# Optimization experiments

Measured on AMD Instinct MI355X. Metric: run time of the kernel, lower is better.

## Reference

```python
import jax, jax.numpy as jnp
import numpy as np

B, S, D, H = 4, 1024, 1024, 16
DK = D // H  # 64


def setup_inputs() -> dict:
    key = jax.random.key(0)
    kx, kq, kk, kv, ko = jax.random.split(key, 5)
    scale = 1.0 / np.sqrt(D)
    x = jax.random.normal(kx, (B, S, D), dtype=jnp.float32)
    # per-head torch nn.Linear weights stacked: [H, d_k, d_model]
    Wq = jax.random.uniform(kq, (H, DK, D), jnp.float32, -scale, scale)
    Wk = jax.random.uniform(kk, (H, DK, D), jnp.float32, -scale, scale)
    Wv = jax.random.uniform(kv, (H, DK, D), jnp.float32, -scale, scale)
    Wo = jax.random.uniform(ko, (D, D), jnp.float32, -scale, scale)  # torch layout [out, in]
    # causal mask, broadcastable to (B, H, S, S); True = keep
    mask = jnp.tril(jnp.ones((S, S), dtype=bool))[None, None]
    return {"x": x, "Wq": Wq, "Wk": Wk, "Wv": Wv, "Wo": Wo, "mask": mask}


def reference(x, Wq, Wk, Wv, Wo, mask):
    # self-attention: context = x. Batched equivalent of the per-head loop.
    Q = jnp.einsum('bsd,hkd->bhsk', x, Wq)  # (B,H,S,DK)
    K = jnp.einsum('bsd,hkd->bhsk', x, Wk)
    V = jnp.einsum('bsd,hkd->bhsk', x, Wv)
    scores = jnp.einsum('bhqd,bhkd->bhqk', Q, K) / jnp.sqrt(jnp.float32(DK))
    scores = jnp.where(mask, scores, jnp.float32(-jnp.inf))
    weights = jax.nn.softmax(scores, axis=-1)  # (B,H,S,S)
    out = jnp.einsum('bhqk,bhkd->bhqd', weights, V)  # (B,H,S,DK)
    # concat heads along feature dim (head order preserved), then W_o
    concat = jnp.swapaxes(out, 1, 2).reshape(B, S, D)
    output = jnp.einsum('bqd,od->bqo', concat, Wo)
    return output, weights
```

## Files before the change

### kernel.cpp

```cpp
#include <hip/hip_runtime.h>
#include <hip/hip_bf16.h>

#define BB 4
#define SS 1024
#define DD 1024
#define HH 16
#define DKK 64

typedef __bf16 bf16;
typedef __bf16 bf16x8 __attribute__((ext_vector_type(8)));
typedef __bf16 bf16x4 __attribute__((ext_vector_type(4)));
typedef float f32x4 __attribute__((ext_vector_type(4)));

#define MFMA(a, b, c) __builtin_amdgcn_mfma_f32_16x16x32_bf16((a), (b), (c), 0, 0, 0)

__device__ __forceinline__ bf16x8 load8(const bf16* p) {
    return *reinterpret_cast<const bf16x8*>(p);
}

__device__ __forceinline__ void gload16(const bf16* g, bf16* l) {
    __builtin_amdgcn_global_load_lds(
        (const __attribute__((address_space(1))) void*)g,
        (__attribute__((address_space(3))) void*)l, 16, 0, 0);
}

__global__ __launch_bounds__(256) void cvt_bf16(const float* __restrict__ x,
                                                const float* __restrict__ Wq,
                                                const float* __restrict__ Wk,
                                                const float* __restrict__ Wv,
                                                const float* __restrict__ Wo,
                                                bf16* __restrict__ dst) {
    const size_t MEG = 1024 * 1024;
    size_t e = ((size_t)blockIdx.x * 256 + threadIdx.x) * 4;
    const float* src;
    size_t off;
    if (e < 4 * MEG)      { src = x;  off = e; }
    else if (e < 5 * MEG) { src = Wq; off = e - 4 * MEG; }
    else if (e < 6 * MEG) { src = Wk; off = e - 5 * MEG; }
    else if (e < 7 * MEG) { src = Wv; off = e - 6 * MEG; }
    else                  { src = Wo; off = e - 7 * MEG; }
    f32x4 v = *reinterpret_cast<const f32x4*>(src + off);
    bf16x4 o;
    o[0] = (bf16)v[0]; o[1] = (bf16)v[1]; o[2] = (bf16)v[2]; o[3] = (bf16)v[3];
    *reinterpret_cast<bf16x4*>(dst + e) = o;
}

template <int MODE>
__global__ __launch_bounds__(256) void gemm128(const bf16* __restrict__ A,
                                               const bf16* __restrict__ Bm,
                                               void* __restrict__ o0,
                                               void* __restrict__ o1,
                                               void* __restrict__ o2) {
    const int lane = threadIdx.x & 63;
    const int wave = threadIdx.x >> 6;
    const int wr = wave >> 1, wc = wave & 1;
    const int m0 = blockIdx.x * 128;
    const int n0 = blockIdx.y * 128;
    const int K = DD;

    __shared__ __align__(16) bf16 As[128][32];
    __shared__ __align__(16) bf16 Bs[128][32];

    const int r0 = wave * 32 + (lane >> 2);
    const int r1 = r0 + 16;
    const int csw = ((lane & 3) ^ (r0 & 3)) * 8;

    const bf16* Ag0 = A + (size_t)(m0 + r0) * K + csw;
    const bf16* Ag1 = A + (size_t)(m0 + r1) * K + csw;
    const bf16* Bg0 = Bm + (size_t)(n0 + r0) * K + csw;
    const bf16* Bg1 = Bm + (size_t)(n0 + r1) * K + csw;
    bf16* Aw0 = &As[wave * 32][0];
    bf16* Aw1 = &As[wave * 32 + 16][0];
    bf16* Bw0 = &Bs[wave * 32][0];
    bf16* Bw1 = &Bs[wave * 32 + 16][0];

    const int rsw = ((lane >> 4) ^ (lane & 3)) * 8;
    const int rrow = lane & 15;

    f32x4 acc[4][4] = {};

    for (int k0 = 0; k0 < K; k0 += 32) {
        __syncthreads();
        gload16(Ag0 + k0, Aw0);
        gload16(Ag1 + k0, Aw1);
        gload16(Bg0 + k0, Bw0);
        gload16(Bg1 + k0, Bw1);
        __syncthreads();
        bf16x8 af[4], bfr[4];
#pragma unroll
        for (int i = 0; i < 4; i++)
            af[i] = *reinterpret_cast<const bf16x8*>(&As[wr * 64 + i * 16 + rrow][rsw]);
#pragma unroll
        for (int j = 0; j < 4; j++)
            bfr[j] = *reinterpret_cast<const bf16x8*>(&Bs[wc * 64 + j * 16 + rrow][rsw]);
#pragma unroll
        for (int i = 0; i < 4; i++)
#pragma unroll
            for (int j = 0; j < 4; j++)
                acc[i][j] = MFMA(af[i], bfr[j], acc[i][j]);
    }

    if constexpr (MODE == 0) {
        bf16* Qo = (bf16*)o0;
        bf16* Ko = (bf16*)o1;
        bf16* Vto = (bf16*)o2;
        const int z = n0 >> 10;
#pragma unroll
        for (int i = 0; i < 4; i++)
#pragma unroll
            for (int j = 0; j < 4; j++)
#pragma unroll
                for (int r = 0; r < 4; r++) {
                    int m = m0 + wr * 64 + i * 16 + (lane >> 4) * 4 + r;
                    int n = n0 + wc * 64 + j * 16 + (lane & 15);
                    int b = m >> 10, s = m & 1023;
                    int nn = n & 1023, h = nn >> 6, dk = nn & 63;
                    bf16 v = (bf16)acc[i][j][r];
                    if (z == 0)
                        Qo[(((size_t)(b * HH + h)) * SS + s) * DKK + dk] = v;
                    else if (z == 1)
                        Ko[(((size_t)(b * HH + h)) * SS + s) * DKK + dk] = v;
                    else
                        Vto[(((size_t)(b * HH + h)) * DKK + dk) * SS + s] = v;
                }
    } else {
        float* Out = (float*)o0;
#pragma unroll
        for (int i = 0; i < 4; i++)
#pragma unroll
            for (int j = 0; j < 4; j++)
#pragma unroll
                for (int r = 0; r < 4; r++) {
                    int m = m0 + wr * 64 + i * 16 + (lane >> 4) * 4 + r;
                    int n = n0 + wc * 64 + j * 16 + (lane & 15);
                    Out[(size_t)m * DD + n] = acc[i][j][r];
                }
    }
}

__global__ __launch_bounds__(256, 4) void attn(const bf16* __restrict__ Q,
                                               const bf16* __restrict__ K,
                                               const bf16* __restrict__ Vt,
                                               float* __restrict__ Wgt,
                                               bf16* __restrict__ Ctx) {
    const int tid = threadIdx.x;
    const int lane = tid & 63;
    const int wave = tid >> 6;
    const int bh = blockIdx.x;
    const int qb = (blockIdx.y + (blockIdx.x & 3)) & 15;
    const int q0 = qb * 64 + wave * 16;
    const int lr = lane & 15;
    const int g = lane >> 4;
    const int lk8 = g * 8;
    const int rbase = g * 4;
    const int own_diag = q0 >> 4;
    const int nch = qb + 1;

    const bf16* Qb = Q + (size_t)bh * SS * DKK;
    const bf16* Kb = K + (size_t)bh * SS * DKK;
    const bf16* Vb = Vt + (size_t)bh * DKK * SS;
    float* Wrow = Wgt + ((size_t)bh * SS + q0) * SS;

    __shared__ __align__(16) bf16 Ks[2][64][64];
    __shared__ __align__(16) bf16 Vs[2][64][64];
    __shared__ __align__(16) bf16 Ps[4][16][40];

    const int skr = tid >> 2;
    const int sc0 = tid & 3;
    const int sw0 = (sc0 ^ (skr & 7)) * 8;
    const int sw1 = ((sc0 + 4) ^ (skr & 7)) * 8;

    bf16x8 qa0 = load8(Qb + (size_t)(q0 + lr) * DKK + lk8);
    bf16x8 qa1 = load8(Qb + (size_t)(q0 + lr) * DKK + 32 + lk8);
#pragma unroll
    for (int i = 0; i < 8; i++) {
        qa0[i] = (bf16)((float)qa0[i] * 0.125f);
        qa1[i] = (bf16)((float)qa1[i] * 0.125f);
    }

    const int rsw0 = (g ^ (lr & 7)) * 8;
    const int rsw1 = ((4 + g) ^ (lr & 7)) * 8;

    float sl[4] = {0.f, 0.f, 0.f, 0.f};

    {
        bf16x8 ka = load8(Kb + (size_t)skr * DKK + sc0 * 8);
        bf16x8 kb_ = load8(Kb + (size_t)skr * DKK + (sc0 + 4) * 8);
        *reinterpret_cast<bf16x8*>(&Ks[0][skr][sw0]) = ka;
        *reinterpret_cast<bf16x8*>(&Ks[0][skr][sw1]) = kb_;
        __syncthreads();
        for (int ch = 0; ch < nch; ch++) {
            const int cur = ch & 1;
            if (ch + 1 < nch) {
                ka = load8(Kb + (size_t)((ch + 1) * 64 + skr) * DKK + sc0 * 8);
                kb_ = load8(Kb + (size_t)((ch + 1) * 64 + skr) * DKK + (sc0 + 4) * 8);
            }
#pragma unroll
            for (int t = 0; t < 4; t++) {
                const int kt = ch * 4 + t;
                if (kt <= own_diag) {
                    bf16x8 kb0 = *reinterpret_cast<const bf16x8*>(&Ks[cur][t * 16 + lr][rsw0]);
                    bf16x8 kb1 = *reinterpret_cast<const bf16x8*>(&Ks[cur][t * 16 + lr][rsw1]);
                    f32x4 sc = {};
                    sc = MFMA(qa0, kb0, sc);
                    sc = MFMA(qa1, kb1, sc);
                    const int kcol = kt * 16 + lr;
#pragma unroll
                    for (int r = 0; r < 4; r++)
                        sl[r] += (kcol <= q0 + rbase + r) ? __expf(sc[r]) : 0.f;
                }
            }
            if (ch + 1 < nch) {
                *reinterpret_cast<bf16x8*>(&Ks[cur ^ 1][skr][sw0]) = ka;
                *reinterpret_cast<bf16x8*>(&Ks[cur ^ 1][skr][sw1]) = kb_;
            }
            __syncthreads();
        }
    }
    float inv[4];
#pragma unroll
    for (int r = 0; r < 4; r++) {
        float t = sl[r];
        t += __shfl_xor(t, 1);
        t += __shfl_xor(t, 2);
        t += __shfl_xor(t, 4);
        t += __shfl_xor(t, 8);
        inv[r] = 1.f / t;
    }

    f32x4 oacc[4] = {};
    {
        bf16x8 ka = load8(Kb + (size_t)skr * DKK + sc0 * 8);
        bf16x8 kb_ = load8(Kb + (size_t)skr * DKK + (sc0 + 4) * 8);
        bf16x8 va = load8(Vb + (size_t)skr * SS + sc0 * 8);
        bf16x8 vb_ = load8(Vb + (size_t)skr * SS + (sc0 + 4) * 8);
        *reinterpret_cast<bf16x8*>(&Ks[0][skr][sw0]) = ka;
        *reinterpret_cast<bf16x8*>(&Ks[0][skr][sw1]) = kb_;
        *reinterpret_cast<bf16x8*>(&Vs[0][skr][sw0]) = va;
        *reinterpret_cast<bf16x8*>(&Vs[0][skr][sw1]) = vb_;
        __syncthreads();
        for (int ch = 0; ch < nch; ch++) {
            const int cur = ch & 1;
            if (ch + 1 < nch) {
                ka = load8(Kb + (size_t)((ch + 1) * 64 + skr) * DKK + sc0 * 8);
                kb_ = load8(Kb + (size_t)((ch + 1) * 64 + skr) * DKK + (sc0 + 4) * 8);
                va = load8(Vb + (size_t)skr * SS + (ch + 1) * 64 + sc0 * 8);
                vb_ = load8(Vb + (size_t)skr * SS + (ch + 1) * 64 + (sc0 + 4) * 8);
            }
#pragma unroll
            for (int t = 0; t < 4; t++) {
                const int kt = ch * 4 + t;
                if (kt <= own_diag) {
                    bf16x8 kb0 = *reinterpret_cast<const bf16x8*>(&Ks[cur][t * 16 + lr][rsw0]);
                    bf16x8 kb1 = *reinterpret_cast<const bf16x8*>(&Ks[cur][t * 16 + lr][rsw1]);
                    f32x4 sc = {};
                    sc = MFMA(qa0, kb0, sc);
                    sc = MFMA(qa1, kb1, sc);
                    const int kcol = kt * 16 + lr;
#pragma unroll
                    for (int r = 0; r < 4; r++) {
                        float p = (kcol <= q0 + rbase + r) ? __expf(sc[r]) * inv[r] : 0.f;
                        Ps[wave][rbase + r][(t & 1) * 16 + lr] = (bf16)p;
                    }
                } else {
#pragma unroll
                    for (int r = 0; r < 4; r++)
                        Ps[wave][rbase + r][(t & 1) * 16 + lr] = (bf16)0.f;
                }
                if (t & 1) {
                    const int colbase = ch * 64 + (t >> 1) * 32;
                    const int prow = lane >> 2;
                    const int pcol = (lane & 3) * 8;
                    bf16x8 pv8 = *reinterpret_cast<const bf16x8*>(&Ps[wave][prow][pcol]);
                    f32x4 w0, w1;
#pragma unroll
                    for (int i = 0; i < 4; i++) {
                        w0[i] = (float)pv8[i];
                        w1[i] = (float)pv8[4 + i];
                    }
                    float* dst = Wrow + (size_t)prow * SS + colbase + pcol;
                    *reinterpret_cast<f32x4*>(dst) = w0;
                    *reinterpret_cast<f32x4*>(dst + 4) = w1;
                    if (kt - 1 <= own_diag) {
                        const int p2 = t >> 1;
                        bf16x8 pf = *reinterpret_cast<const bf16x8*>(&Ps[wave][lr][lk8]);
#pragma unroll
                        for (int j = 0; j < 4; j++) {
                            bf16x8 vb = *reinterpret_cast<const bf16x8*>(
                                &Vs[cur][j * 16 + lr][((4 * p2 + g) ^ (lr & 7)) * 8]);
                            oacc[j] = MFMA(pf, vb, oacc[j]);
                        }
                    }
                }
            }
            if (ch + 1 < nch) {
                *reinterpret_cast<bf16x8*>(&Ks[cur ^ 1][skr][sw0]) = ka;
                *reinterpret_cast<bf16x8*>(&Ks[cur ^ 1][skr][sw1]) = kb_;
                *reinterpret_cast<bf16x8*>(&Vs[cur ^ 1][skr][sw0]) = va;
                *reinterpret_cast<bf16x8*>(&Vs[cur ^ 1][skr][sw1]) = vb_;
            }
            __syncthreads();
        }
    }

    const int b = bh >> 4, h = bh & 15;
#pragma unroll
    for (int j = 0; j < 4; j++)
#pragma unroll
        for (int r = 0; r < 4; r++) {
            int qrow = q0 + rbase + r;
            int col = h * 64 + j * 16 + lr;
            Ctx[((size_t)b * SS + qrow) * DD + col] = (bf16)oacc[j][r];
        }

    const int zc0 = nch * 64;
    if (zc0 < SS) {
        const int nc4 = (SS - zc0) >> 2;
        float* zbase = Wgt + ((size_t)bh * SS + qb * 64) * SS + zc0;
        const f32x4 z = {0.f, 0.f, 0.f, 0.f};
        for (int r = 0; r < 64; r++)
            for (int c = tid; c < nc4; c += 256)
                reinterpret_cast<f32x4*>(zbase + (size_t)r * SS)[c] = z;
    }
}

extern "C" void kernel_launch(void* const* d_in, const int* in_sizes, int n_in,
                              void* d_out, int out_size, void* d_ws, size_t ws_size,
                              hipStream_t stream) {
    const float* x  = (const float*)d_in[0];
    const float* Wq = (const float*)d_in[1];
    const float* Wk = (const float*)d_in[2];
    const float* Wv = (const float*)d_in[3];
    const float* Wo = (const float*)d_in[4];

    float* out = (float*)d_out;
    float* wgt = out + (size_t)BB * SS * DD;

    const size_t MEG = 1024 * 1024;
    bf16* xb   = (bf16*)d_ws;
    bf16* wcat = xb + 4 * MEG;
    bf16* wob  = xb + 7 * MEG;
    bf16* qws  = xb + 8 * MEG;
    bf16* kws  = xb + 12 * MEG;
    bf16* vws  = xb + 16 * MEG;
    bf16* cws  = xb + 20 * MEG;

    cvt_bf16<<<dim3(8192), 256, 0, stream>>>(x, Wq, Wk, Wv, Wo, xb);
    gemm128<0><<<dim3(32, 24), 256, 0, stream>>>(xb, wcat, qws, kws, vws);
    attn<<<dim3(64, 16), 256, 0, stream>>>(qws, kws, vws, wgt, cws);
    gemm128<1><<<dim3(32, 8), 256, 0, stream>>>(cws, wob, out, nullptr, nullptr);
}
```

Before: 146.3 us.

## Double GEMM K-tile to 64 and interleave causal zero-fill with first attention pass

```diff
diff --git a/kernel.cpp b/kernel.cpp
--- a/kernel.cpp
+++ b/kernel.cpp
@@ -58,46 +58,53 @@
     const int n0 = blockIdx.y * 128;
     const int K = DD;
 
-    __shared__ __align__(16) bf16 As[128][32];
-    __shared__ __align__(16) bf16 Bs[128][32];
-
-    const int r0 = wave * 32 + (lane >> 2);
-    const int r1 = r0 + 16;
-    const int csw = ((lane & 3) ^ (r0 & 3)) * 8;
-
-    const bf16* Ag0 = A + (size_t)(m0 + r0) * K + csw;
-    const bf16* Ag1 = A + (size_t)(m0 + r1) * K + csw;
-    const bf16* Bg0 = Bm + (size_t)(n0 + r0) * K + csw;
-    const bf16* Bg1 = Bm + (size_t)(n0 + r1) * K + csw;
-    bf16* Aw0 = &As[wave * 32][0];
-    bf16* Aw1 = &As[wave * 32 + 16][0];
-    bf16* Bw0 = &Bs[wave * 32][0];
-    bf16* Bw1 = &Bs[wave * 32 + 16][0];
-
-    const int rsw = ((lane >> 4) ^ (lane & 3)) * 8;
+    __shared__ __align__(16) bf16 As[128][64];
+    __shared__ __align__(16) bf16 Bs[128][64];
+
+    const int srow = lane >> 3;
+    const int csw = ((lane & 7) ^ srow) * 8;
+
+    const bf16 *Ag[4], *Bg[4];
+    bf16 *Aw[4], *Bw[4];
+#pragma unroll
+    for (int q = 0; q < 4; q++) {
+        const int rr = wave * 32 + q * 8;
+        Ag[q] = A + (size_t)(m0 + rr + srow) * K + csw;
+        Bg[q] = Bm + (size_t)(n0 + rr + srow) * K + csw;
+        Aw[q] = &As[rr][0];
+        Bw[q] = &Bs[rr][0];
+    }
+
     const int rrow = lane & 15;
+    const int g = lane >> 4;
+    const int rs0 = (g ^ (rrow & 7)) * 8;
+    const int rs1 = ((4 + g) ^ (rrow & 7)) * 8;
 
     f32x4 acc[4][4] = {};
 
-    for (int k0 = 0; k0 < K; k0 += 32) {
+    for (int k0 = 0; k0 < K; k0 += 64) {
         __syncthreads();
-        gload16(Ag0 + k0, Aw0);
-        gload16(Ag1 + k0, Aw1);
-        gload16(Bg0 + k0, Bw0);
-        gload16(Bg1 + k0, Bw1);
+#pragma unroll
+        for (int q = 0; q < 4; q++) gload16(Ag[q] + k0, Aw[q]);
+#pragma unroll
+        for (int q = 0; q < 4; q++) gload16(Bg[q] + k0, Bw[q]);
         __syncthreads();
-        bf16x8 af[4], bfr[4];
-#pragma unroll
-        for (int i = 0; i < 4; i++)
-            af[i] = *reinterpret_cast<const bf16x8*>(&As[wr * 64 + i * 16 + rrow][rsw]);
-#pragma unroll
-        for (int j = 0; j < 4; j++)
-            bfr[j] = *reinterpret_cast<const bf16x8*>(&Bs[wc * 64 + j * 16 + rrow][rsw]);
-#pragma unroll
-        for (int i = 0; i < 4; i++)
+#pragma unroll
+        for (int half = 0; half < 2; half++) {
+            const int rs = half ? rs1 : rs0;
+            bf16x8 af[4], bfr[4];
+#pragma unroll
+            for (int i = 0; i < 4; i++)
+                af[i] = *reinterpret_cast<const bf16x8*>(&As[wr * 64 + i * 16 + rrow][rs]);
 #pragma unroll
             for (int j = 0; j < 4; j++)
-                acc[i][j] = MFMA(af[i], bfr[j], acc[i][j]);
+                bfr[j] = *reinterpret_cast<const bf16x8*>(&Bs[wc * 64 + j * 16 + rrow][rs]);
+#pragma unroll
+            for (int i = 0; i < 4; i++)
+#pragma unroll
+                for (int j = 0; j < 4; j++)
+                    acc[i][j] = MFMA(af[i], bfr[j], acc[i][j]);
+        }
     }
 
     if constexpr (MODE == 0) {
@@ -181,6 +188,14 @@
     const int rsw0 = (g ^ (lr & 7)) * 8;
     const int rsw1 = ((4 + g) ^ (lr & 7)) * 8;
 
+    const int nz4 = 256 - nch * 16;
+    const int npt = nz4 >> 2;
+    const int npc = (npt + nch - 1) / nch;
+    float* zptr = Wgt + ((size_t)bh * SS + qb * 64 + (tid >> 2)) * SS
+                + nch * 64 + (tid & 3) * 4;
+    const f32x4 z4 = {0.f, 0.f, 0.f, 0.f};
+    int zj = 0;
+
     float sl[4] = {0.f, 0.f, 0.f, 0.f};
 
     {
@@ -194,6 +209,11 @@
             if (ch + 1 < nch) {
                 ka = load8(Kb + (size_t)((ch + 1) * 64 + skr) * DKK + sc0 * 8);
                 kb_ = load8(Kb + (size_t)((ch + 1) * 64 + skr) * DKK + (sc0 + 4) * 8);
+            }
+            {
+                const int zend = (zj + npc < npt) ? zj + npc : npt;
+                for (; zj < zend; zj++)
+                    *reinterpret_cast<f32x4*>(zptr + zj * 16) = z4;
             }
 #pragma unroll
             for (int t = 0; t < 4; t++) {
@@ -312,16 +332,6 @@
             int col = h * 64 + j * 16 + lr;
             Ctx[((size_t)b * SS + qrow) * DD + col] = (bf16)oacc[j][r];
         }
-
-    const int zc0 = nch * 64;
-    if (zc0 < SS) {
-        const int nc4 = (SS - zc0) >> 2;
-        float* zbase = Wgt + ((size_t)bh * SS + qb * 64) * SS + zc0;
-        const f32x4 z = {0.f, 0.f, 0.f, 0.f};
-        for (int r = 0; r < 64; r++)
-            for (int c = tid; c < nc4; c += 256)
-                reinterpret_cast<f32x4*>(zbase + (size_t)r * SS)[c] = z;
-    }
 }
 
 extern "C" void kernel_launch(void* const* d_in, const int* in_sizes, int n_in,
```

Result: slower. 152.6 us (+4.3%).

## Fuse fp32-to-bf16 conversion into GEMM loads with register prefetch

Applied to the files above, without the earlier changes.

```diff
diff --git a/kernel.cpp b/kernel.cpp
--- a/kernel.cpp
+++ b/kernel.cpp
@@ -18,36 +18,20 @@
     return *reinterpret_cast<const bf16x8*>(p);
 }
 
-__device__ __forceinline__ void gload16(const bf16* g, bf16* l) {
-    __builtin_amdgcn_global_load_lds(
-        (const __attribute__((address_space(1))) void*)g,
-        (__attribute__((address_space(3))) void*)l, 16, 0, 0);
-}
-
-__global__ __launch_bounds__(256) void cvt_bf16(const float* __restrict__ x,
-                                                const float* __restrict__ Wq,
-                                                const float* __restrict__ Wk,
-                                                const float* __restrict__ Wv,
-                                                const float* __restrict__ Wo,
-                                                bf16* __restrict__ dst) {
-    const size_t MEG = 1024 * 1024;
-    size_t e = ((size_t)blockIdx.x * 256 + threadIdx.x) * 4;
-    const float* src;
-    size_t off;
-    if (e < 4 * MEG)      { src = x;  off = e; }
-    else if (e < 5 * MEG) { src = Wq; off = e - 4 * MEG; }
-    else if (e < 6 * MEG) { src = Wk; off = e - 5 * MEG; }
-    else if (e < 7 * MEG) { src = Wv; off = e - 6 * MEG; }
-    else                  { src = Wo; off = e - 7 * MEG; }
-    f32x4 v = *reinterpret_cast<const f32x4*>(src + off);
-    bf16x4 o;
-    o[0] = (bf16)v[0]; o[1] = (bf16)v[1]; o[2] = (bf16)v[2]; o[3] = (bf16)v[3];
-    *reinterpret_cast<bf16x4*>(dst + e) = o;
+__device__ __forceinline__ bf16x8 load8f(const float* p) {
+    f32x4 a = *reinterpret_cast<const f32x4*>(p);
+    f32x4 b = *reinterpret_cast<const f32x4*>(p + 4);
+    bf16x8 o;
+    o[0] = (bf16)a[0]; o[1] = (bf16)a[1]; o[2] = (bf16)a[2]; o[3] = (bf16)a[3];
+    o[4] = (bf16)b[0]; o[5] = (bf16)b[1]; o[6] = (bf16)b[2]; o[7] = (bf16)b[3];
+    return o;
 }
 
 template <int MODE>
-__global__ __launch_bounds__(256) void gemm128(const bf16* __restrict__ A,
-                                               const bf16* __restrict__ Bm,
+__global__ __launch_bounds__(256) void gemm128(const void* __restrict__ Av,
+                                               const float* __restrict__ W0,
+                                               const float* __restrict__ W1,
+                                               const float* __restrict__ W2,
                                                void* __restrict__ o0,
                                                void* __restrict__ o1,
                                                void* __restrict__ o2) {
@@ -61,31 +45,64 @@
     __shared__ __align__(16) bf16 As[128][32];
     __shared__ __align__(16) bf16 Bs[128][32];
 
-    const int r0 = wave * 32 + (lane >> 2);
-    const int r1 = r0 + 16;
-    const int csw = ((lane & 3) ^ (r0 & 3)) * 8;
-
-    const bf16* Ag0 = A + (size_t)(m0 + r0) * K + csw;
-    const bf16* Ag1 = A + (size_t)(m0 + r1) * K + csw;
-    const bf16* Bg0 = Bm + (size_t)(n0 + r0) * K + csw;
-    const bf16* Bg1 = Bm + (size_t)(n0 + r1) * K + csw;
-    bf16* Aw0 = &As[wave * 32][0];
-    bf16* Aw1 = &As[wave * 32 + 16][0];
-    bf16* Bw0 = &Bs[wave * 32][0];
-    bf16* Bw1 = &Bs[wave * 32 + 16][0];
+    const int srow = threadIdx.x >> 2;
+    const int schk = threadIdx.x & 3;
+    const int swz = (schk ^ (srow & 3)) * 8;
+
+    const int z = n0 >> 10;
+    const int nn0 = n0 & 1023;
+    const float* W = (z == 0) ? W0 : ((z == 1) ? W1 : W2);
+
+    const float* Bg0 = W + (size_t)(nn0 + srow) * K + schk * 8;
+    const float* Bg1 = Bg0 + (size_t)64 * K;
+
+    bf16* Aw0 = &As[srow][swz];
+    bf16* Aw1 = &As[srow + 64][swz];
+    bf16* Bw0 = &Bs[srow][swz];
+    bf16* Bw1 = &Bs[srow + 64][swz];
 
     const int rsw = ((lane >> 4) ^ (lane & 3)) * 8;
     const int rrow = lane & 15;
 
     f32x4 acc[4][4] = {};
 
+    const float* Agf0 = nullptr;
+    const float* Agf1 = nullptr;
+    const bf16* Agb0 = nullptr;
+    const bf16* Agb1 = nullptr;
+    bf16x8 ra0, ra1, rb0, rb1;
+    if constexpr (MODE == 0) {
+        Agf0 = (const float*)Av + (size_t)(m0 + srow) * K + schk * 8;
+        Agf1 = Agf0 + (size_t)64 * K;
+        ra0 = load8f(Agf0);
+        ra1 = load8f(Agf1);
+    } else {
+        Agb0 = (const bf16*)Av + (size_t)(m0 + srow) * K + schk * 8;
+        Agb1 = Agb0 + (size_t)64 * K;
+        ra0 = load8(Agb0);
+        ra1 = load8(Agb1);
+    }
+    rb0 = load8f(Bg0);
+    rb1 = load8f(Bg1);
+
     for (int k0 = 0; k0 < K; k0 += 32) {
         __syncthreads();
-        gload16(Ag0 + k0, Aw0);
-        gload16(Ag1 + k0, Aw1);
-        gload16(Bg0 + k0, Bw0);
-        gload16(Bg1 + k0, Bw1);
+        *reinterpret_cast<bf16x8*>(Aw0) = ra0;
+        *reinterpret_cast<bf16x8*>(Aw1) = ra1;
+        *reinterpret_cast<bf16x8*>(Bw0) = rb0;
+        *reinterpret_cast<bf16x8*>(Bw1) = rb1;
         __syncthreads();
+        if (k0 + 32 < K) {
+            if constexpr (MODE == 0) {
+                ra0 = load8f(Agf0 + k0 + 32);
+                ra1 = load8f(Agf1 + k0 + 32);
+            } else {
+                ra0 = load8(Agb0 + k0 + 32);
+                ra1 = load8(Agb1 + k0 + 32);
+            }
+            rb0 = load8f(Bg0 + k0 + 32);
+            rb1 = load8f(Bg1 + k0 + 32);
+        }
         bf16x8 af[4], bfr[4];
 #pragma unroll
         for (int i = 0; i < 4; i++)
@@ -104,7 +121,6 @@
         bf16* Qo = (bf16*)o0;
         bf16* Ko = (bf16*)o1;
         bf16* Vto = (bf16*)o2;
-        const int z = n0 >> 10;
 #pragma unroll
         for (int i = 0; i < 4; i++)
 #pragma unroll
@@ -337,16 +353,13 @@
     float* wgt = out + (size_t)BB * SS * DD;
 
     const size_t MEG = 1024 * 1024;
-    bf16* xb   = (bf16*)d_ws;
-    bf16* wcat = xb + 4 * MEG;
-    bf16* wob  = xb + 7 * MEG;
-    bf16* qws  = xb + 8 * MEG;
-    bf16* kws  = xb + 12 * MEG;
-    bf16* vws  = xb + 16 * MEG;
-    bf16* cws  = xb + 20 * MEG;
-
-    cvt_bf16<<<dim3(8192), 256, 0, stream>>>(x, Wq, Wk, Wv, Wo, xb);
-    gemm128<0><<<dim3(32, 24), 256, 0, stream>>>(xb, wcat, qws, kws, vws);
+    bf16* qws = (bf16*)d_ws;
+    bf16* kws = qws + 4 * MEG;
+    bf16* vws = kws + 4 * MEG;
+    bf16* cws = vws + 4 * MEG;
+
+    gemm128<0><<<dim3(32, 24), 256, 0, stream>>>(x, Wq, Wk, Wv, qws, kws, vws);
     attn<<<dim3(64, 16), 256, 0, stream>>>(qws, kws, vws, wgt, cws);
-    gemm128<1><<<dim3(32, 8), 256, 0, stream>>>(cws, wob, out, nullptr, nullptr);
-}
+    gemm128<1><<<dim3(32, 8), 256, 0, stream>>>(cws, Wo, nullptr, nullptr,
+                                                out, nullptr, nullptr);
+}
```

Result: slower. 164.0 us (+12.0%).
